# Performance work log

Measured on AMD Instinct MI355X. Metric: run time of the kernel, lower is better.

The kernel has to match this reference:

```python
import jax, jax.numpy as jnp
import numpy as np

EMBED_DIM = 1024
NUM_HEADS = 16
HEAD_DIM = EMBED_DIM // NUM_HEADS
EPS = 1e-5


def setup_inputs() -> dict:
    key = jax.random.key(0)
    ks = jax.random.split(key, 14)
    B, S, E = 2, 2048, EMBED_DIM
    s = 1.0 / np.sqrt(E)
    inp = {
        "x": jax.random.normal(ks[0], (B, S, E), dtype=jnp.float32),
        "Wq": jax.random.normal(ks[1], (E, E), dtype=jnp.float32) * s,
        "bq": jax.random.normal(ks[2], (E,), dtype=jnp.float32) * 0.01,
        "Wk": jax.random.normal(ks[3], (E, E), dtype=jnp.float32) * s,
        "bk": jax.random.normal(ks[4], (E,), dtype=jnp.float32) * 0.01,
        "Wv": jax.random.normal(ks[5], (E, E), dtype=jnp.float32) * s,
        "bv": jax.random.normal(ks[6], (E,), dtype=jnp.float32) * 0.01,
        "Wo": jax.random.normal(ks[7], (E, E), dtype=jnp.float32) * s,
        "bo": jax.random.normal(ks[8], (E,), dtype=jnp.float32) * 0.01,
        "qn_w": jnp.ones((HEAD_DIM,), jnp.float32) + 0.1 * jax.random.normal(ks[9], (HEAD_DIM,), jnp.float32),
        "qn_b": 0.1 * jax.random.normal(ks[10], (HEAD_DIM,), jnp.float32),
        "kn_w": jnp.ones((HEAD_DIM,), jnp.float32) + 0.1 * jax.random.normal(ks[11], (HEAD_DIM,), jnp.float32),
        "kn_b": 0.1 * jax.random.normal(ks[12], (HEAD_DIM,), jnp.float32),
    }
    return inp


def _layernorm(t, w, b):
    # normalize over last axis (head_dim), matching eqx.nn.LayerNorm(eps=1e-5)
    mu = jnp.mean(t, axis=-1, keepdims=True)
    var = jnp.mean(jnp.square(t - mu), axis=-1, keepdims=True)
    return (t - mu) * jax.lax.rsqrt(var + EPS) * w + b


def reference(x, Wq, bq, Wk, bk, Wv, bv, Wo, bo, qn_w, qn_b, kn_w, kn_b):
    B, S, E = x.shape
    H, D = NUM_HEADS, HEAD_DIM
    q = (x @ Wq.T + bq).reshape(B, S, H, D)
    k = (x @ Wk.T + bk).reshape(B, S, H, D)
    v = (x @ Wv.T + bv).reshape(B, S, H, D)
    q = _layernorm(q, qn_w, qn_b)
    k = _layernorm(k, kn_w, kn_b)
    scale = D ** (-0.5)
    # [B,H,S,S] score matrix (faithful to naive implementation)
    scores = jnp.einsum("bqhd,bkhd->bhqk", q, k) * scale
    attn = jax.nn.softmax(scores, axis=-1)
    out = jnp.einsum("bhqk,bkhd->bqhd", attn, v).reshape(B, S, E)
    return out @ Wo.T + bo
```

## Files before the change

kernel.cpp:

```cpp
#include <hip/hip_runtime.h>
#include <stdint.h>


typedef __bf16 bf16_t;
typedef __bf16 bf16x8 __attribute__((ext_vector_type(8)));
typedef __bf16 bf16x4 __attribute__((ext_vector_type(4)));
typedef __bf16 bf16x2 __attribute__((ext_vector_type(2)));
typedef float f32x4 __attribute__((ext_vector_type(4)));
typedef float f32x16 __attribute__((ext_vector_type(16)));
typedef uint32_t u32x4 __attribute__((ext_vector_type(4)));

#define S_LEN 2048

__device__ __forceinline__ void load_lds16(const void* g, void* l) {
  __builtin_amdgcn_global_load_lds((__attribute__((address_space(1))) void*)g,
                                   (__attribute__((address_space(3))) void*)l,
                                   16, 0, 0);
}

__device__ __forceinline__ f32x4 mfma16(bf16x8 a, bf16x8 b, f32x4 c) {
  return __builtin_amdgcn_mfma_f32_16x16x32_bf16(a, b, c, 0, 0, 0);
}

__device__ __forceinline__ f32x16 mfma32(bf16x8 a, bf16x8 b, f32x16 c) {
  return __builtin_amdgcn_mfma_f32_32x32x16_bf16(a, b, c, 0, 0, 0);
}

__device__ __forceinline__ uint32_t pk_bf16(float a, float b) {
  bf16x2 v; v[0] = (bf16_t)a; v[1] = (bf16_t)b;
  return __builtin_bit_cast(uint32_t, v);
}

__device__ __forceinline__ void plswap(uint32_t& a, uint32_t& b) {
  asm volatile("v_permlane32_swap_b32 %0, %1" : "+v"(a), "+v"(b));
}

__global__ void cvt_all(const float* __restrict__ x, const float* __restrict__ Wq,
                        const float* __restrict__ Wk, const float* __restrict__ Wv,
                        const float* __restrict__ Wo,
                        bf16_t* __restrict__ xb, bf16_t* __restrict__ Wb,
                        bf16_t* __restrict__ Wob) {
  const int bid = blockIdx.x;
  const float* src; bf16_t* dst; int idx;
  if (bid < 4096) { src = x; dst = xb; idx = bid; }
  else {
    const int r = bid - 4096, rg = r >> 10;
    idx = r & 1023;
    if (rg == 0)      { src = Wq; dst = Wb; }
    else if (rg == 1) { src = Wk; dst = Wb + (1 << 20); }
    else if (rg == 2) { src = Wv; dst = Wb + (2 << 20); }
    else              { src = Wo; dst = Wob; }
  }
  const int i = (idx * 256 + threadIdx.x) * 4;
  float4 v = *reinterpret_cast<const float4*>(src + i);
  bf16x4 o;
  o[0] = (bf16_t)v.x; o[1] = (bf16_t)v.y; o[2] = (bf16_t)v.z; o[3] = (bf16_t)v.w;
  *reinterpret_cast<bf16x4*>(dst + i) = o;
}

__device__ __forceinline__ void gemm_main(const bf16_t* __restrict__ ga,
                                          const bf16_t* __restrict__ gb,
                                          bf16_t* As, bf16_t* Bs,
                                          int t, int wr, int wc, int lg, int lr,
                                          f32x4 (&acc)[4][4]) {
  for (int k0 = 0; k0 < 1024; k0 += 32) {
    load_lds16(ga + k0,          As + t * 8);
    load_lds16(ga + 65536 + k0,  As + 2048 + t * 8);
    load_lds16(gb + k0,          Bs + t * 8);
    load_lds16(gb + 65536 + k0,  Bs + 2048 + t * 8);
    __syncthreads();
    bf16x8 af[4], bfr[4];
#pragma unroll
    for (int mt = 0; mt < 4; ++mt)
      af[mt] = *reinterpret_cast<const bf16x8*>(As + ((wr * 64 + mt * 16 + lr) << 5) + lg * 8);
#pragma unroll
    for (int nt = 0; nt < 4; ++nt)
      bfr[nt] = *reinterpret_cast<const bf16x8*>(Bs + ((wc * 64 + nt * 16 + lr) << 5) + lg * 8);
#pragma unroll
    for (int mt = 0; mt < 4; ++mt)
#pragma unroll
      for (int nt = 0; nt < 4; ++nt)
        acc[mt][nt] = mfma16(af[mt], bfr[nt], acc[mt][nt]);
    __syncthreads();
  }
}

__launch_bounds__(256, 2)
__global__ void gemm_qkv_ln(const bf16_t* __restrict__ A, const bf16_t* __restrict__ Bt,
                            const float* __restrict__ bq, const float* __restrict__ bk,
                            const float* __restrict__ bv,
                            const float* __restrict__ qnw, const float* __restrict__ qnb,
                            const float* __restrict__ knw, const float* __restrict__ knb,
                            bf16_t* __restrict__ Qb, bf16_t* __restrict__ Kb,
                            bf16_t* __restrict__ Vt) {
  __shared__ alignas(16) bf16_t As[128 * 32];
  __shared__ alignas(16) bf16_t Bs[128 * 32];
  const int t = threadIdx.x;
  const int bm = blockIdx.y, bn = blockIdx.x;
  const int w = t >> 6, lane = t & 63;
  const int wr = w >> 1, wc = w & 1;
  const int lg = lane >> 4, lr = lane & 15;

  f32x4 acc[4][4] = {};
  const int srow = t >> 2;
  const int scol = (t & 3) << 3;
  const bf16_t* ga = A + ((size_t)(bm * 128 + srow) << 10) + scol;
  const bf16_t* gb = Bt + ((size_t)(bn * 128 + srow) << 10) + scol;
  gemm_main(ga, gb, As, Bs, t, wr, wc, lg, lr, acc);

  const int nbase = bn * 128 + wc * 64;
  const int region = nbase >> 10;
  const int h = (nbase & 1023) >> 6;

  if (region == 2) {
#pragma unroll
    for (int mt = 0; mt < 4; ++mt)
#pragma unroll
      for (int r = 0; r < 4; ++r) {
        const int gm = bm * 128 + wr * 64 + mt * 16 + lg * 4 + r;
        const int b = gm >> 11, s = gm & 2047;
#pragma unroll
        for (int nt = 0; nt < 4; ++nt) {
          const int d = nt * 16 + lr;
          float val = acc[mt][nt][r] + bv[h * 64 + d];
          Vt[((size_t)((b * 16 + h) * 64 + d) << 11) + s] = (bf16_t)val;
        }
      }
  } else {
    const float* bias = region ? bk : bq;
    const float* lw = region ? knw : qnw;
    const float* lb = region ? knb : qnb;
    bf16_t* Outp = region ? Kb : Qb;
#pragma unroll
    for (int mt = 0; mt < 4; ++mt)
#pragma unroll
      for (int r = 0; r < 4; ++r) {
        const int gm = bm * 128 + wr * 64 + mt * 16 + lg * 4 + r;
        const int b = gm >> 11, s = gm & 2047;
        float vv[4], sum = 0.f, sumsq = 0.f;
#pragma unroll
        for (int nt = 0; nt < 4; ++nt) {
          const int d = nt * 16 + lr;
          vv[nt] = acc[mt][nt][r] + bias[h * 64 + d];
          sum += vv[nt];
          sumsq += vv[nt] * vv[nt];
        }
#pragma unroll
        for (int mk = 1; mk < 16; mk <<= 1) {
          sum += __shfl_xor(sum, mk);
          sumsq += __shfl_xor(sumsq, mk);
        }
        const float mean = sum * (1.f / 64.f);
        const float var = sumsq * (1.f / 64.f) - mean * mean;
        const float rstd = rsqrtf(var + 1e-5f);
        const size_t rowoff = ((size_t)((b * 16 + h) * 2048 + s)) << 6;
#pragma unroll
        for (int nt = 0; nt < 4; ++nt) {
          const int d = nt * 16 + lr;
          float y = (vv[nt] - mean) * rstd * lw[d] + lb[d];
          Outp[rowoff + d] = (bf16_t)y;
        }
      }
  }
}

__launch_bounds__(256, 2)
__global__ void gemm_out(const bf16_t* __restrict__ A, const bf16_t* __restrict__ Bt,
                         const float* __restrict__ bo, float* __restrict__ dout) {
  __shared__ alignas(16) bf16_t As[64 * 32];
  __shared__ alignas(16) bf16_t Bs[128 * 32];
  const int t = threadIdx.x;
  const int bm = blockIdx.y, bn = blockIdx.x;
  const int w = t >> 6, lane = t & 63;
  const int wr = w >> 1, wc = w & 1;
  const int lg = lane >> 4, lr = lane & 15;

  f32x4 acc[2][4] = {};
  const int srow = t >> 2;
  const int scol = (t & 3) << 3;
  const bf16_t* ga = A + ((size_t)(bm * 64 + srow) << 10) + scol;
  const bf16_t* gb = Bt + ((size_t)(bn * 128 + srow) << 10) + scol;

  for (int k0 = 0; k0 < 1024; k0 += 32) {
    load_lds16(ga + k0,          As + t * 8);
    load_lds16(gb + k0,          Bs + t * 8);
    load_lds16(gb + 65536 + k0,  Bs + 2048 + t * 8);
    __syncthreads();
    bf16x8 af[2], bfr[4];
#pragma unroll
    for (int mt = 0; mt < 2; ++mt)
      af[mt] = *reinterpret_cast<const bf16x8*>(As + ((wr * 32 + mt * 16 + lr) << 5) + lg * 8);
#pragma unroll
    for (int nt = 0; nt < 4; ++nt)
      bfr[nt] = *reinterpret_cast<const bf16x8*>(Bs + ((wc * 64 + nt * 16 + lr) << 5) + lg * 8);
#pragma unroll
    for (int mt = 0; mt < 2; ++mt)
#pragma unroll
      for (int nt = 0; nt < 4; ++nt)
        acc[mt][nt] = mfma16(af[mt], bfr[nt], acc[mt][nt]);
    __syncthreads();
  }

#pragma unroll
  for (int mt = 0; mt < 2; ++mt)
#pragma unroll
    for (int r = 0; r < 4; ++r) {
      const int gm = bm * 64 + wr * 32 + mt * 16 + lg * 4 + r;
#pragma unroll
      for (int nt = 0; nt < 4; ++nt) {
        const int gn = bn * 128 + wc * 64 + nt * 16 + lr;
        dout[((size_t)gm << 10) + gn] = acc[mt][nt][r] + bo[gn];
      }
    }
}

template <int NSPLIT>
__launch_bounds__(256, 4)
__global__ void attn_kernel(const bf16_t* __restrict__ Qb, const bf16_t* __restrict__ Kb,
                            const bf16_t* __restrict__ Vt, bf16_t* __restrict__ Og,
                            float* __restrict__ Op, float* __restrict__ Ml) {
  __shared__ alignas(16) bf16_t KVs[4][64 * 64];

  const int t = threadIdx.x;
  const int w = t >> 6, lane = t & 63;
  const int lq = lane & 31;
  const int hi = lane >> 5;
  const int bh = blockIdx.y;
  const int z = (NSPLIT == 1) ? 0 : blockIdx.z;
  const int b = bh >> 4, h = bh & 15;
  const int q0 = blockIdx.x * 128 + w * 32;
  const int ntiles = 32 / NSPLIT;

  bf16x8 qf[4];
  {
    const bf16_t* qp = Qb + (((size_t)bh * S_LEN + q0 + lq) << 6) + hi * 8;
#pragma unroll
    for (int c = 0; c < 4; ++c)
      qf[c] = *reinterpret_cast<const bf16x8*>(qp + c * 16);
  }

  f32x16 oacc0 = {}, oacc1 = {};
  float m_ = -1e30f, l_ = 0.f;
  const float sc = 0.125f * 1.44269504f;

  const int sr = t >> 3;
  const int ssw = ((t & 7) ^ (sr & 7)) << 3;
  const bf16_t* kbase = Kb + (((size_t)bh * S_LEN) << 6);
  const bf16_t* vbase = Vt + ((size_t)bh << 17);

#define STAGE(buf, jt)                                                       \
  {                                                                          \
    const bf16_t* kb = kbase + ((size_t)((jt) * 64) << 6);                   \
    const bf16_t* vb = vbase + (jt) * 64;                                    \
    load_lds16(kb + (sr << 6) + ssw,        &KVs[buf][t * 8]);               \
    load_lds16(kb + ((sr + 32) << 6) + ssw, &KVs[buf][2048 + t * 8]);        \
    load_lds16(vb + sr * S_LEN + ssw,        &KVs[2 + (buf)][t * 8]);        \
    load_lds16(vb + (sr + 32) * S_LEN + ssw, &KVs[2 + (buf)][2048 + t * 8]); \
  }

  STAGE(0, z * ntiles);
  __syncthreads();

  for (int j = 0; j < ntiles; ++j) {
    const int cur = j & 1;
    if (j < ntiles - 1) STAGE(cur ^ 1, z * ntiles + j + 1);

    f32x16 sa0, sa1;
    {
      f32x16 z0 = {}, z1 = {};
      const int row0 = lq, row1 = 32 + lq;
      const bf16_t* kr0 = &KVs[cur][row0 << 6];
      const bf16_t* kr1 = &KVs[cur][row1 << 6];
      const int sw0 = row0 & 7, sw1 = row1 & 7;
#pragma unroll
      for (int c = 0; c < 4; ++c) {
        bf16x8 kf0 = *reinterpret_cast<const bf16x8*>(kr0 + (((c * 2 + hi) ^ sw0) << 3));
        z0 = mfma32(kf0, qf[c], z0);
      }
#pragma unroll
      for (int c = 0; c < 4; ++c) {
        bf16x8 kf1 = *reinterpret_cast<const bf16x8*>(kr1 + (((c * 2 + hi) ^ sw1) << 3));
        z1 = mfma32(kf1, qf[c], z1);
      }
      sa0 = z0; sa1 = z1;
    }

    float mv[16];
#pragma unroll
    for (int i = 0; i < 16; ++i) mv[i] = fmaxf(sa0[i], sa1[i]);
#pragma unroll
    for (int s2 = 8; s2 >= 1; s2 >>= 1)
#pragma unroll
      for (int i = 0; i < s2; ++i) mv[i] = fmaxf(mv[i], mv[i + s2]);
    float mx = fmaxf(mv[0], __shfl_xor(mv[0], 32));
    const float ms = mx * sc;

    if (__any(ms > m_ + 8.f)) {
      const float mn = fmaxf(m_, ms);
      const float alpha = __builtin_amdgcn_exp2f(m_ - mn);
      oacc0 *= alpha; oacc1 *= alpha;
      l_ *= alpha;
      m_ = mn;
    }

    const float mneg = -m_;
    f32x16 p0, p1;
#pragma unroll
    for (int i = 0; i < 16; ++i) p0[i] = __builtin_amdgcn_exp2f(__builtin_fmaf(sa0[i], sc, mneg));
#pragma unroll
    for (int i = 0; i < 16; ++i) p1[i] = __builtin_amdgcn_exp2f(__builtin_fmaf(sa1[i], sc, mneg));

    float sv[16];
#pragma unroll
    for (int i = 0; i < 16; ++i) sv[i] = p0[i] + p1[i];
#pragma unroll
    for (int s2 = 8; s2 >= 1; s2 >>= 1)
#pragma unroll
      for (int i = 0; i < s2; ++i) sv[i] += sv[i + s2];
    l_ += sv[0] + __shfl_xor(sv[0], 32);

#pragma unroll
    for (int c = 0; c < 4; ++c) {
      const f32x16 ph = (c < 2) ? p0 : p1;
      const int cl = c & 1;
      uint32_t w00 = pk_bf16(ph[8 * cl + 0], ph[8 * cl + 1]);
      uint32_t w01 = pk_bf16(ph[8 * cl + 2], ph[8 * cl + 3]);
      uint32_t w10 = pk_bf16(ph[8 * cl + 4], ph[8 * cl + 5]);
      uint32_t w11 = pk_bf16(ph[8 * cl + 6], ph[8 * cl + 7]);
      plswap(w00, w10);
      plswap(w01, w11);
      u32x4 pw = {w00, w01, w10, w11};
      bf16x8 pf = __builtin_bit_cast(bf16x8, pw);
      {
        const int vrow = lq;
        bf16x8 vf = *reinterpret_cast<const bf16x8*>(
            &KVs[2 + cur][(vrow << 6) + (((c * 2 + hi) ^ (vrow & 7)) << 3)]);
        oacc0 = mfma32(vf, pf, oacc0);
      }
      {
        const int vrow = 32 + lq;
        bf16x8 vf = *reinterpret_cast<const bf16x8*>(
            &KVs[2 + cur][(vrow << 6) + (((c * 2 + hi) ^ (vrow & 7)) << 3)]);
        oacc1 = mfma32(vf, pf, oacc1);
      }
    }
    __syncthreads();
  }

  if constexpr (NSPLIT == 1) {
    bf16_t* Os = &KVs[0][0] + w * 2048;
    const float inv = __builtin_amdgcn_rcpf(l_);
#pragma unroll
    for (int dh = 0; dh < 2; ++dh) {
      const f32x16 oa = dh ? oacc1 : oacc0;
#pragma unroll
      for (int g = 0; g < 8; ++g) {
        const int reg = g * 2;
        const int dl = (reg & 3) + 8 * (reg >> 2) + 4 * hi;
        const int d = dh * 32 + dl;
        const uint32_t wv = pk_bf16(oa[reg] * inv, oa[reg + 1] * inv);
        const int byte = lq * 128 + ((((d >> 3) ^ (lq & 7))) << 4) + ((d & 7) << 1);
        *reinterpret_cast<uint32_t*>(reinterpret_cast<char*>(Os) + byte) = wv;
      }
    }
#pragma unroll
    for (int it = 0; it < 4; ++it) {
      const int q = it * 8 + (lane >> 3);
      const int ch = lane & 7;
      bf16x8 ov = *reinterpret_cast<const bf16x8*>(
          reinterpret_cast<char*>(Os) + q * 128 + ((ch ^ (q & 7)) << 4));
      const size_t gaddr = (((size_t)(b * S_LEN + q0 + q)) << 10) + h * 64 + ch * 8;
      *reinterpret_cast<bf16x8*>(Og + gaddr) = ov;
    }
  } else {
    float* Os32 = reinterpret_cast<float*>(&KVs[0][0]) + w * 2048;
#pragma unroll
    for (int dh = 0; dh < 2; ++dh) {
      const f32x16 oa = dh ? oacc1 : oacc0;
#pragma unroll
      for (int reg = 0; reg < 16; ++reg) {
        const int dl = (reg & 3) + 8 * (reg >> 2) + 4 * hi;
        const int d = dh * 32 + dl;
        Os32[lq * 64 + (((d >> 2) ^ (lq & 15)) << 2) + (d & 3)] = oa[reg];
      }
    }
    if (lane < 32) {
      float2 mlv; mlv.x = m_; mlv.y = l_;
      *reinterpret_cast<float2*>(Ml + (((size_t)(z * 32 + bh) * 2048 + q0 + lq) << 1)) = mlv;
    }
#pragma unroll
    for (int it = 0; it < 4; ++it) {
      const int q = it * 8 + (lane >> 3);
      const size_t rowoff = ((size_t)((z * 32 + bh) * 2048 + q0 + q)) << 6;
#pragma unroll
      for (int c2 = 0; c2 < 2; ++c2) {
        const int ch = ((lane & 7) << 1) + c2;
        f32x4 v = *reinterpret_cast<const f32x4*>(Os32 + q * 64 + ((ch ^ (q & 15)) << 2));
        *reinterpret_cast<f32x4*>(Op + rowoff + (ch << 2)) = v;
      }
    }
  }
#undef STAGE
}

__global__ void attn_combine(const float* __restrict__ Op, const float* __restrict__ Ml,
                             bf16_t* __restrict__ Ob) {
  const int gid = blockIdx.x * 256 + threadIdx.x;
  const int row = gid >> 4, ch = gid & 15;
  const float* o1 = Op + ((size_t)row << 6) + ch * 4;
  const float* o2 = o1 + (1u << 22);
  const float2 a1 = *reinterpret_cast<const float2*>(Ml + row * 2);
  const float2 a2 = *reinterpret_cast<const float2*>(Ml + (1u << 17) + row * 2);
  const float mmax = fmaxf(a1.x, a2.x);
  const float w1 = __builtin_amdgcn_exp2f(a1.x - mmax);
  const float w2 = __builtin_amdgcn_exp2f(a2.x - mmax);
  const float inv = 1.f / (a1.y * w1 + a2.y * w2);
  f32x4 v1 = *reinterpret_cast<const f32x4*>(o1);
  f32x4 v2 = *reinterpret_cast<const f32x4*>(o2);
  bf16x4 o;
#pragma unroll
  for (int i = 0; i < 4; ++i) o[i] = (bf16_t)((v1[i] * w1 + v2[i] * w2) * inv);
  const int bh = row >> 11, s = row & 2047;
  const int b = bh >> 4, h = bh & 15;
  *reinterpret_cast<bf16x4*>(Ob + (((size_t)(b * S_LEN + s)) << 10) + h * 64 + ch * 4) = o;
}

extern "C" void kernel_launch(void* const* d_in, const int* in_sizes, int n_in,
                              void* d_out, int out_size, void* d_ws, size_t ws_size,
                              hipStream_t stream) {
  const float* x = (const float*)d_in[0];
  const float* Wq = (const float*)d_in[1];
  const float* bq = (const float*)d_in[2];
  const float* Wk = (const float*)d_in[3];
  const float* bk = (const float*)d_in[4];
  const float* Wv = (const float*)d_in[5];
  const float* bv = (const float*)d_in[6];
  const float* Wo = (const float*)d_in[7];
  const float* bo = (const float*)d_in[8];
  const float* qnw = (const float*)d_in[9];
  const float* qnb = (const float*)d_in[10];
  const float* knw = (const float*)d_in[11];
  const float* knb = (const float*)d_in[12];
  float* out = (float*)d_out;

  uint8_t* ws = (uint8_t*)d_ws;
  bf16_t* xb = (bf16_t*)(ws + 0);
  bf16_t* Wb = (bf16_t*)(ws + 8388608);
  bf16_t* Wob = (bf16_t*)(ws + 14680064);
  bf16_t* Qb = (bf16_t*)(ws + 16777216);
  bf16_t* Kb = (bf16_t*)(ws + 25165824);
  bf16_t* Vt = (bf16_t*)(ws + 33554432);
  bf16_t* Ob = (bf16_t*)(ws + 41943040);
  float*  Opart = (float*)(ws + 50331648);
  float*  Mlp   = (float*)(ws + 83886080);
  const bool split = ws_size >= 84934656ull;

  cvt_all<<<8192, 256, 0, stream>>>(x, Wq, Wk, Wv, Wo, xb, Wb, Wob);

  gemm_qkv_ln<<<dim3(24, 32), 256, 0, stream>>>(xb, Wb, bq, bk, bv, qnw, qnb, knw, knb,
                                                Qb, Kb, Vt);
  if (split) {
    attn_kernel<2><<<dim3(16, 32, 2), 256, 0, stream>>>(Qb, Kb, Vt, Ob, Opart, Mlp);
    attn_combine<<<4096, 256, 0, stream>>>(Opart, Mlp, Ob);
  } else {
    attn_kernel<1><<<dim3(16, 32, 1), 256, 0, stream>>>(Qb, Kb, Vt, Ob, Opart, Mlp);
  }
  gemm_out<<<dim3(8, 64), 256, 0, stream>>>(Ob, Wob, bo, out);
}
```

Before: 131.6 us.

## Drop online softmax max tracking, fold scale into Q, remap block order

The attention loop no longer tracks a running maximum or rescales its accumulators. It relies on Q and K being layer-normalized, which keeps the scores small enough for a direct exp2 in fp32. The softmax scale and log2e are folded into Q in the QKV GEMM epilogue, and row sums are accumulated per lane and reduced once after the loop. With no max to merge, the split-K combine reduces to adding the partial sums. The K/V shared-memory staging layout is also changed to drop the XOR swizzle, and all three main kernels remap block IDs so consecutive blocks land on the same XCD. The risk is overflow if the layernorm weights produce large scores, plus possible LDS bank conflicts from the new unswizzled layout.

```diff
diff --git a/kernel.cpp b/kernel.cpp
--- a/kernel.cpp
+++ b/kernel.cpp
@@ -11,6 +11,7 @@
 typedef uint32_t u32x4 __attribute__((ext_vector_type(4)));
 
 #define S_LEN 2048
+#define QSCALE 0.1803368801f
 
 __device__ __forceinline__ void load_lds16(const void* g, void* l) {
   __builtin_amdgcn_global_load_lds((__attribute__((address_space(1))) void*)g,
@@ -96,7 +97,9 @@
   __shared__ alignas(16) bf16_t As[128 * 32];
   __shared__ alignas(16) bf16_t Bs[128 * 32];
   const int t = threadIdx.x;
-  const int bm = blockIdx.y, bn = blockIdx.x;
+  const int orig = blockIdx.y * 24 + blockIdx.x;
+  const int logical = (orig & 7) * 96 + (orig >> 3);
+  const int bn = logical % 24, bm = logical / 24;
   const int w = t >> 6, lane = t & 63;
   const int wr = w >> 1, wc = w & 1;
   const int lg = lane >> 4, lr = lane & 15;
@@ -130,6 +133,7 @@
     const float* bias = region ? bk : bq;
     const float* lw = region ? knw : qnw;
     const float* lb = region ? knb : qnb;
+    const float osc = region ? 1.0f : QSCALE;
     bf16_t* Outp = region ? Kb : Qb;
 #pragma unroll
     for (int mt = 0; mt < 4; ++mt)
@@ -157,7 +161,7 @@
 #pragma unroll
         for (int nt = 0; nt < 4; ++nt) {
           const int d = nt * 16 + lr;
-          float y = (vv[nt] - mean) * rstd * lw[d] + lb[d];
+          float y = ((vv[nt] - mean) * rstd * lw[d] + lb[d]) * osc;
           Outp[rowoff + d] = (bf16_t)y;
         }
       }
@@ -170,7 +174,9 @@
   __shared__ alignas(16) bf16_t As[64 * 32];
   __shared__ alignas(16) bf16_t Bs[128 * 32];
   const int t = threadIdx.x;
-  const int bm = blockIdx.y, bn = blockIdx.x;
+  const int orig = blockIdx.y * 8 + blockIdx.x;
+  const int logical = (orig & 7) * 64 + (orig >> 3);
+  const int bn = logical & 7, bm = logical >> 3;
   const int w = t >> 6, lane = t & 63;
   const int wr = w >> 1, wc = w & 1;
   const int lg = lane >> 4, lr = lane & 15;
@@ -218,17 +224,20 @@
 __launch_bounds__(256, 4)
 __global__ void attn_kernel(const bf16_t* __restrict__ Qb, const bf16_t* __restrict__ Kb,
                             const bf16_t* __restrict__ Vt, bf16_t* __restrict__ Og,
-                            float* __restrict__ Op, float* __restrict__ Ml) {
+                            float* __restrict__ Op, float* __restrict__ Lp) {
   __shared__ alignas(16) bf16_t KVs[4][64 * 64];
 
   const int t = threadIdx.x;
   const int w = t >> 6, lane = t & 63;
   const int lq = lane & 31;
   const int hi = lane >> 5;
-  const int bh = blockIdx.y;
-  const int z = (NSPLIT == 1) ? 0 : blockIdx.z;
+  const int orig = (blockIdx.z * 32 + blockIdx.y) * 16 + blockIdx.x;
+  const int logical = (orig & 7) * (64 * NSPLIT) + (orig >> 3);
+  const int qt = logical & 15;
+  const int bh = (logical >> 4) & 31;
+  const int z = (NSPLIT == 1) ? 0 : (logical >> 9);
   const int b = bh >> 4, h = bh & 15;
-  const int q0 = blockIdx.x * 128 + w * 32;
+  const int q0 = qt * 128 + w * 32;
   const int ntiles = 32 / NSPLIT;
 
   bf16x8 qf[4];
@@ -239,23 +248,21 @@
       qf[c] = *reinterpret_cast<const bf16x8*>(qp + c * 16);
   }
 
-  f32x16 oacc0 = {}, oacc1 = {};
-  float m_ = -1e30f, l_ = 0.f;
-  const float sc = 0.125f * 1.44269504f;
-
-  const int sr = t >> 3;
-  const int ssw = ((t & 7) ^ (sr & 7)) << 3;
-  const bf16_t* kbase = Kb + (((size_t)bh * S_LEN) << 6);
-  const bf16_t* vbase = Vt + ((size_t)bh << 17);
+  f32x16 oacc0 = {}, oacc1 = {}, lacc = {};
+
+  const int krow = (t >> 1) & 63;
+  const int kch = ((t >> 7) << 1) | (t & 1);
+  const bf16_t* kbase = Kb + (((size_t)bh * S_LEN) << 6) + krow * 64 + kch * 8;
+  const bf16_t* vbase = Vt + ((size_t)bh << 17) + krow * S_LEN + kch * 8;
 
 #define STAGE(buf, jt)                                                       \
   {                                                                          \
-    const bf16_t* kb = kbase + ((size_t)((jt) * 64) << 6);                   \
-    const bf16_t* vb = vbase + (jt) * 64;                                    \
-    load_lds16(kb + (sr << 6) + ssw,        &KVs[buf][t * 8]);               \
-    load_lds16(kb + ((sr + 32) << 6) + ssw, &KVs[buf][2048 + t * 8]);        \
-    load_lds16(vb + sr * S_LEN + ssw,        &KVs[2 + (buf)][t * 8]);        \
-    load_lds16(vb + (sr + 32) * S_LEN + ssw, &KVs[2 + (buf)][2048 + t * 8]); \
+    const bf16_t* kb_ = kbase + (((size_t)(jt)) << 12);                      \
+    const bf16_t* vb_ = vbase + (jt) * 64;                                   \
+    load_lds16(kb_,      &KVs[buf][t * 8]);                                  \
+    load_lds16(kb_ + 32, &KVs[buf][2048 + t * 8]);                           \
+    load_lds16(vb_,      &KVs[2 + (buf)][t * 8]);                            \
+    load_lds16(vb_ + 32, &KVs[2 + (buf)][2048 + t * 8]);                     \
   }
 
   STAGE(0, z * ntiles);
@@ -265,60 +272,28 @@
     const int cur = j & 1;
     if (j < ntiles - 1) STAGE(cur ^ 1, z * ntiles + j + 1);
 
-    f32x16 sa0, sa1;
-    {
-      f32x16 z0 = {}, z1 = {};
-      const int row0 = lq, row1 = 32 + lq;
-      const bf16_t* kr0 = &KVs[cur][row0 << 6];
-      const bf16_t* kr1 = &KVs[cur][row1 << 6];
-      const int sw0 = row0 & 7, sw1 = row1 & 7;
-#pragma unroll
-      for (int c = 0; c < 4; ++c) {
-        bf16x8 kf0 = *reinterpret_cast<const bf16x8*>(kr0 + (((c * 2 + hi) ^ sw0) << 3));
-        z0 = mfma32(kf0, qf[c], z0);
-      }
-#pragma unroll
-      for (int c = 0; c < 4; ++c) {
-        bf16x8 kf1 = *reinterpret_cast<const bf16x8*>(kr1 + (((c * 2 + hi) ^ sw1) << 3));
-        z1 = mfma32(kf1, qf[c], z1);
-      }
-      sa0 = z0; sa1 = z1;
-    }
-
-    float mv[16];
-#pragma unroll
-    for (int i = 0; i < 16; ++i) mv[i] = fmaxf(sa0[i], sa1[i]);
-#pragma unroll
-    for (int s2 = 8; s2 >= 1; s2 >>= 1)
-#pragma unroll
-      for (int i = 0; i < s2; ++i) mv[i] = fmaxf(mv[i], mv[i + s2]);
-    float mx = fmaxf(mv[0], __shfl_xor(mv[0], 32));
-    const float ms = mx * sc;
-
-    if (__any(ms > m_ + 8.f)) {
-      const float mn = fmaxf(m_, ms);
-      const float alpha = __builtin_amdgcn_exp2f(m_ - mn);
-      oacc0 *= alpha; oacc1 *= alpha;
-      l_ *= alpha;
-      m_ = mn;
-    }
-
-    const float mneg = -m_;
+    f32x16 s0 = {}, s1 = {};
+    const bf16_t* kr = &KVs[cur][lq * 16 + hi * 8];
+#pragma unroll
+    for (int c = 0; c < 4; ++c) {
+      bf16x8 kf = *reinterpret_cast<const bf16x8*>(kr + c * 1024);
+      s0 = mfma32(kf, qf[c], s0);
+    }
+#pragma unroll
+    for (int c = 0; c < 4; ++c) {
+      bf16x8 kf = *reinterpret_cast<const bf16x8*>(kr + 512 + c * 1024);
+      s1 = mfma32(kf, qf[c], s1);
+    }
+
     f32x16 p0, p1;
 #pragma unroll
-    for (int i = 0; i < 16; ++i) p0[i] = __builtin_amdgcn_exp2f(__builtin_fmaf(sa0[i], sc, mneg));
-#pragma unroll
-    for (int i = 0; i < 16; ++i) p1[i] = __builtin_amdgcn_exp2f(__builtin_fmaf(sa1[i], sc, mneg));
-
-    float sv[16];
-#pragma unroll
-    for (int i = 0; i < 16; ++i) sv[i] = p0[i] + p1[i];
-#pragma unroll
-    for (int s2 = 8; s2 >= 1; s2 >>= 1)
-#pragma unroll
-      for (int i = 0; i < s2; ++i) sv[i] += sv[i + s2];
-    l_ += sv[0] + __shfl_xor(sv[0], 32);
-
+    for (int i = 0; i < 16; ++i) p0[i] = __builtin_amdgcn_exp2f(s0[i]);
+#pragma unroll
+    for (int i = 0; i < 16; ++i) p1[i] = __builtin_amdgcn_exp2f(s1[i]);
+    lacc += p0;
+    lacc += p1;
+
+    const bf16_t* vr = &KVs[2 + cur][lq * 16 + hi * 8];
 #pragma unroll
     for (int c = 0; c < 4; ++c) {
       const f32x16 ph = (c < 2) ? p0 : p1;
@@ -332,19 +307,27 @@
       u32x4 pw = {w00, w01, w10, w11};
       bf16x8 pf = __builtin_bit_cast(bf16x8, pw);
       {
-        const int vrow = lq;
-        bf16x8 vf = *reinterpret_cast<const bf16x8*>(
-            &KVs[2 + cur][(vrow << 6) + (((c * 2 + hi) ^ (vrow & 7)) << 3)]);
+        bf16x8 vf = *reinterpret_cast<const bf16x8*>(vr + c * 1024);
         oacc0 = mfma32(vf, pf, oacc0);
       }
       {
-        const int vrow = 32 + lq;
-        bf16x8 vf = *reinterpret_cast<const bf16x8*>(
-            &KVs[2 + cur][(vrow << 6) + (((c * 2 + hi) ^ (vrow & 7)) << 3)]);
+        bf16x8 vf = *reinterpret_cast<const bf16x8*>(vr + 512 + c * 1024);
         oacc1 = mfma32(vf, pf, oacc1);
       }
     }
     __syncthreads();
+  }
+
+  float l_;
+  {
+    float sv[8];
+#pragma unroll
+    for (int i = 0; i < 8; ++i) sv[i] = lacc[i] + lacc[i + 8];
+#pragma unroll
+    for (int s2 = 4; s2 >= 1; s2 >>= 1)
+#pragma unroll
+      for (int i = 0; i < s2; ++i) sv[i] += sv[i + s2];
+    l_ = sv[0] + __shfl_xor(sv[0], 32);
   }
 
   if constexpr (NSPLIT == 1) {
@@ -384,10 +367,7 @@
         Os32[lq * 64 + (((d >> 2) ^ (lq & 15)) << 2) + (d & 3)] = oa[reg];
       }
     }
-    if (lane < 32) {
-      float2 mlv; mlv.x = m_; mlv.y = l_;
-      *reinterpret_cast<float2*>(Ml + (((size_t)(z * 32 + bh) * 2048 + q0 + lq) << 1)) = mlv;
-    }
+    if (lane < 32) Lp[(size_t)(z * 32 + bh) * 2048 + q0 + lq] = l_;
 #pragma unroll
     for (int it = 0; it < 4; ++it) {
       const int q = it * 8 + (lane >> 3);
@@ -403,23 +383,18 @@
 #undef STAGE
 }
 
-__global__ void attn_combine(const float* __restrict__ Op, const float* __restrict__ Ml,
+__global__ void attn_combine(const float* __restrict__ Op, const float* __restrict__ Lp,
                              bf16_t* __restrict__ Ob) {
   const int gid = blockIdx.x * 256 + threadIdx.x;
   const int row = gid >> 4, ch = gid & 15;
   const float* o1 = Op + ((size_t)row << 6) + ch * 4;
   const float* o2 = o1 + (1u << 22);
-  const float2 a1 = *reinterpret_cast<const float2*>(Ml + row * 2);
-  const float2 a2 = *reinterpret_cast<const float2*>(Ml + (1u << 17) + row * 2);
-  const float mmax = fmaxf(a1.x, a2.x);
-  const float w1 = __builtin_amdgcn_exp2f(a1.x - mmax);
-  const float w2 = __builtin_amdgcn_exp2f(a2.x - mmax);
-  const float inv = 1.f / (a1.y * w1 + a2.y * w2);
+  const float inv = 1.f / (Lp[row] + Lp[(1u << 16) + row]);
   f32x4 v1 = *reinterpret_cast<const f32x4*>(o1);
   f32x4 v2 = *reinterpret_cast<const f32x4*>(o2);
   bf16x4 o;
 #pragma unroll
-  for (int i = 0; i < 4; ++i) o[i] = (bf16_t)((v1[i] * w1 + v2[i] * w2) * inv);
+  for (int i = 0; i < 4; ++i) o[i] = (bf16_t)((v1[i] + v2[i]) * inv);
   const int bh = row >> 11, s = row & 2047;
   const int b = bh >> 4, h = bh & 15;
   *reinterpret_cast<bf16x4*>(Ob + (((size_t)(b * S_LEN + s)) << 10) + h * 64 + ch * 4) = o;
@@ -452,7 +427,7 @@
   bf16_t* Vt = (bf16_t*)(ws + 33554432);
   bf16_t* Ob = (bf16_t*)(ws + 41943040);
   float*  Opart = (float*)(ws + 50331648);
-  float*  Mlp   = (float*)(ws + 83886080);
+  float*  Lpart = (float*)(ws + 83886080);
   const bool split = ws_size >= 84934656ull;
 
   cvt_all<<<8192, 256, 0, stream>>>(x, Wq, Wk, Wv, Wo, xb, Wb, Wob);
@@ -460,10 +435,10 @@
   gemm_qkv_ln<<<dim3(24, 32), 256, 0, stream>>>(xb, Wb, bq, bk, bv, qnw, qnb, knw, knb,
                                                 Qb, Kb, Vt);
   if (split) {
-    attn_kernel<2><<<dim3(16, 32, 2), 256, 0, stream>>>(Qb, Kb, Vt, Ob, Opart, Mlp);
-    attn_combine<<<4096, 256, 0, stream>>>(Opart, Mlp, Ob);
+    attn_kernel<2><<<dim3(16, 32, 2), 256, 0, stream>>>(Qb, Kb, Vt, Ob, Opart, Lpart);
+    attn_combine<<<4096, 256, 0, stream>>>(Opart, Lpart, Ob);
   } else {
-    attn_kernel<1><<<dim3(16, 32, 1), 256, 0, stream>>>(Qb, Kb, Vt, Ob, Opart, Mlp);
+    attn_kernel<1><<<dim3(16, 32, 1), 256, 0, stream>>>(Qb, Kb, Vt, Ob, Opart, Lpart);
   }
   gemm_out<<<dim3(8, 64), 256, 0, stream>>>(Ob, Wob, bo, out);
 }
```

Measured after the change: 122.3 us. 7.1% less time.
